# Kernel optimization log

Measured on AMD Instinct MI355X. Metric: run time of the kernel, lower is better.

## Reference

```python
import jax, jax.numpy as jnp
import numpy as np

EPS_RMS = 1e-6  # mmfreelm RMSNorm default eps

def _rmsnorm(x, w):
    var = jnp.mean(x * x, axis=-1, keepdims=True)
    return x * jax.lax.rsqrt(var + EPS_RMS) * w

def _activation_quant(x):
    # per-token absmax int8 quant (BitNet b1.58 activation quant)
    scale = 127.0 / jnp.clip(jnp.max(jnp.abs(x), axis=-1, keepdims=True), 1e-5)
    return jnp.clip(jnp.round(x * scale), -128.0, 127.0) / scale

def _weight_quant(w):
    # ternary quant with global mean-abs scale
    scale = 1.0 / jnp.clip(jnp.mean(jnp.abs(w)), 1e-5)
    return jnp.clip(jnp.round(w * scale), -1.0, 1.0) / scale

def _nm_mask(w, n, m):
    # keep top-n by |w| in every group of m along the input (last) dim
    O, I = w.shape
    g = jnp.abs(w).reshape(-1, m)            # [G, m]
    _, idx = jax.lax.top_k(g, n)             # [G, n]
    rows = jnp.arange(g.shape[0])[:, None]
    mask = jnp.zeros_like(g).at[rows, idx].set(1.0)
    return mask.reshape(O, I)

def setup_inputs() -> dict:
    key = jax.random.key(0)
    k1, k2 = jax.random.split(key)
    B, S, IN, OUT = 4, 2048, 4096, 11008
    x = jax.random.normal(k1, (B, S, IN), dtype=jnp.float32)
    weight = jax.random.normal(k2, (OUT, IN), dtype=jnp.float32) * 0.02
    norm_weight = jnp.ones((IN,), dtype=jnp.float32)
    return {"x": x, "weight": weight, "norm_weight": norm_weight,
            "sparse_n": 2, "sparse_m": 4}

def reference(x, weight, norm_weight, sparse_n, sparse_m):
    x_norm = _rmsnorm(x, norm_weight)
    # STE quantization (forward value == quantized value)
    x_q = x_norm + jax.lax.stop_gradient(_activation_quant(x_norm) - x_norm)
    w_q = weight + jax.lax.stop_gradient(_weight_quant(weight) - weight)
    mask = jax.lax.stop_gradient(_nm_mask(w_q, sparse_n, sparse_m))
    w_sparse = w_q * mask                    # [OUT, IN]
    return jnp.einsum('bsi,oi->bso', x_q, w_sparse)
```

## Files before the change

### kernel.cpp

```cpp
#include <hip/hip_runtime.h>
#include <stdint.h>

#define IN_DIM 4096
#define OUT_DIM 11008
#define TOKENS 8192
#define WN (45088768L)
#define NKT64 64

typedef int int4v __attribute__((ext_vector_type(4)));

__device__ __forceinline__ float bf2f(uint32_t u16) {
  union { uint32_t i; float f; } v; v.i = u16 << 16; return v.f;
}
__device__ __forceinline__ bool probe_bf16(const void* nw) {
  return ((const uint16_t*)nw)[0] == 0x3F80u;
}

__global__ __launch_bounds__(256) void k_wabs(const void* __restrict__ wv,
                                              const void* __restrict__ nwv,
                                              double* __restrict__ partial) {
  const bool b16 = probe_bf16(nwv);
  const long tid = (long)blockIdx.x * 256 + threadIdx.x;
  const long stride = (long)gridDim.x * 256;
  double s = 0.0;
  if (b16) {
    const uint4* w = (const uint4*)wv;
    for (long i = tid; i < WN / 8; i += stride) {
      uint4 v = w[i];
      uint32_t a[4] = {v.x, v.y, v.z, v.w};
      float t = 0.f;
#pragma unroll
      for (int j = 0; j < 4; j++)
        t += fabsf(bf2f(a[j] & 0xffffu)) + fabsf(bf2f(a[j] >> 16));
      s += (double)t;
    }
  } else {
    const float4* w = (const float4*)wv;
    for (long i = tid; i < WN / 4; i += stride) {
      float4 v = w[i];
      s += (double)(fabsf(v.x) + fabsf(v.y) + fabsf(v.z) + fabsf(v.w));
    }
  }
#pragma unroll
  for (int off = 32; off > 0; off >>= 1) s += __shfl_down(s, off);
  __shared__ double sd[4];
  if ((threadIdx.x & 63) == 0) sd[threadIdx.x >> 6] = s;
  __syncthreads();
  if (threadIdx.x == 0) partial[blockIdx.x] = (sd[0] + sd[1]) + (sd[2] + sd[3]);
}

__global__ __launch_bounds__(256) void k_wscale(const double* __restrict__ partial,
                                                float* __restrict__ hdr) {
  double s = 0.0;
  for (int i = threadIdx.x; i < 2048; i += 256) s += partial[i];
#pragma unroll
  for (int off = 32; off > 0; off >>= 1) s += __shfl_down(s, off);
  __shared__ double sd[4];
  if ((threadIdx.x & 63) == 0) sd[threadIdx.x >> 6] = s;
  __syncthreads();
  if (threadIdx.x == 0) {
    double mean = ((sd[0] + sd[1]) + (sd[2] + sd[3])) / (double)WN;
    float meanc = (float)mean;
    if (meanc < 1e-5f) meanc = 1e-5f;
    float wscale = 1.0f / meanc;
    hdr[0] = wscale;
    hdr[1] = 1.0f / wscale;
  }
}

__global__ __launch_bounds__(256) void k_act(const void* __restrict__ xv,
                                             const void* __restrict__ nwv,
                                             int8_t* __restrict__ qxp,
                                             float* __restrict__ invsx) {
  const bool b16 = probe_bf16(nwv);
  const int t = blockIdx.x;
  const int tx = threadIdx.x;
  float xw[16];
  float ss = 0.f, mx = 0.f;
  if (b16) {
    const uint16_t* xr = (const uint16_t*)xv + (long)t * IN_DIM;
    const uint16_t* nw = (const uint16_t*)nwv;
#pragma unroll
    for (int c = 0; c < 2; c++) {
      uint4 vx = ((const uint4*)xr)[tx * 2 + c];
      uint4 vn = ((const uint4*)nw)[tx * 2 + c];
      uint32_t ax[4] = {vx.x, vx.y, vx.z, vx.w};
      uint32_t an[4] = {vn.x, vn.y, vn.z, vn.w};
#pragma unroll
      for (int j = 0; j < 4; j++) {
        float x0 = bf2f(ax[j] & 0xffffu), x1 = bf2f(ax[j] >> 16);
        float n0 = bf2f(an[j] & 0xffffu), n1 = bf2f(an[j] >> 16);
        ss += x0 * x0 + x1 * x1;
        float p0 = x0 * n0, p1 = x1 * n1;
        xw[c * 8 + j * 2]     = p0;
        xw[c * 8 + j * 2 + 1] = p1;
        mx = fmaxf(mx, fmaxf(fabsf(p0), fabsf(p1)));
      }
    }
  } else {
    const float* xr = (const float*)xv + (long)t * IN_DIM;
    const float* nw = (const float*)nwv;
#pragma unroll
    for (int c = 0; c < 4; c++) {
      float4 vx = ((const float4*)xr)[tx * 4 + c];
      float4 vn = ((const float4*)nw)[tx * 4 + c];
      ss += vx.x * vx.x + vx.y * vx.y + vx.z * vx.z + vx.w * vx.w;
      float p0 = vx.x * vn.x, p1 = vx.y * vn.y, p2 = vx.z * vn.z, p3 = vx.w * vn.w;
      xw[c * 4 + 0] = p0; xw[c * 4 + 1] = p1; xw[c * 4 + 2] = p2; xw[c * 4 + 3] = p3;
      mx = fmaxf(mx, fmaxf(fmaxf(fabsf(p0), fabsf(p1)), fmaxf(fabsf(p2), fabsf(p3))));
    }
  }
#pragma unroll
  for (int off = 32; off > 0; off >>= 1) {
    ss += __shfl_down(ss, off);
    mx = fmaxf(mx, __shfl_down(mx, off));
  }
  __shared__ float s_ss[4], s_mx[4];
  __shared__ float bc[1];
  if ((tx & 63) == 0) { s_ss[tx >> 6] = ss; s_mx[tx >> 6] = mx; }
  __syncthreads();
  if (tx == 0) {
    float sst = (s_ss[0] + s_ss[1]) + (s_ss[2] + s_ss[3]);
    float mxt = fmaxf(fmaxf(s_mx[0], s_mx[1]), fmaxf(s_mx[2], s_mx[3]));
    float var = sst / (float)IN_DIM;
    float rms = 1.0f / sqrtf(var + 1e-6f);
    float amax = rms * mxt;
    if (amax < 1e-5f) amax = 1e-5f;
    float scale = 127.0f / amax;
    bc[0] = rms * scale;
    invsx[t] = 1.0f / scale;
  }
  __syncthreads();
  float rsc = bc[0];
  uint32_t pw[4];
#pragma unroll
  for (int d = 0; d < 4; d++) {
    uint32_t v = 0;
#pragma unroll
    for (int j = 0; j < 4; j++) {
      float q = rintf(xw[d * 4 + j] * rsc);
      q = fminf(fmaxf(q, -128.f), 127.f);
      int qi = (int)q;
      v |= ((uint32_t)(qi & 0xff)) << (8 * j);
    }
    pw[d] = v;
  }
  uint4 st; st.x = pw[0]; st.y = pw[1]; st.z = pw[2]; st.w = pw[3];
  const long u4 = (((long)(t >> 7) * 64 + (tx >> 2)) * 8 + ((t >> 4) & 7)) * 64
                + (t & 15) + (tx & 3) * 16;
  ((uint4*)qxp)[u4] = st;
}

__global__ __launch_bounds__(256) void k_wq(const void* __restrict__ wv,
                                            const void* __restrict__ nwv,
                                            const float* __restrict__ hdr,
                                            int8_t* __restrict__ qwp) {
  const bool b16 = probe_bf16(nwv);
  const int o = blockIdx.x;
  const int tx = threadIdx.x;
  const float wscale = hdr[0];
  float f[16];
  if (b16) {
    const uint4* w = (const uint4*)wv;
#pragma unroll
    for (int c = 0; c < 2; ++c) {
      uint4 v = w[(long)o * 512 + tx * 2 + c];
      uint32_t a[4] = {v.x, v.y, v.z, v.w};
#pragma unroll
      for (int j = 0; j < 4; ++j) {
        f[c * 8 + j * 2]     = bf2f(a[j] & 0xffffu);
        f[c * 8 + j * 2 + 1] = bf2f(a[j] >> 16);
      }
    }
  } else {
    const float4* w = (const float4*)wv;
#pragma unroll
    for (int c = 0; c < 4; ++c) {
      float4 v = w[(long)o * 1024 + tx * 4 + c];
      f[c * 4 + 0] = v.x; f[c * 4 + 1] = v.y; f[c * 4 + 2] = v.z; f[c * 4 + 3] = v.w;
    }
  }
  int q[16];
#pragma unroll
  for (int j = 0; j < 16; ++j) {
    float qf = rintf(f[j] * wscale);
    qf = fminf(fmaxf(qf, -1.f), 1.f);
    q[j] = (int)qf;
  }
#pragma unroll
  for (int g = 0; g < 4; ++g) {
    int cnt = 0;
#pragma unroll
    for (int j = 0; j < 4; ++j) {
      int idx = g * 4 + j;
      if (q[idx] != 0) { cnt++; if (cnt > 2) q[idx] = 0; }
    }
  }
  uint32_t pw[4];
#pragma unroll
  for (int d = 0; d < 4; ++d) {
    uint32_t v = 0;
#pragma unroll
    for (int j = 0; j < 4; ++j) v |= ((uint32_t)(q[d * 4 + j] & 0xff)) << (8 * j);
    pw[d] = v;
  }
  uint4 st; st.x = pw[0]; st.y = pw[1]; st.z = pw[2]; st.w = pw[3];
  const long u4 = (((long)(o >> 6) * 64 + (tx >> 2)) * 4 + ((o >> 4) & 3)) * 64
                + (o & 15) + (tx & 3) * 16;
  ((uint4*)qwp)[u4] = st;
}

__global__ __launch_bounds__(512, 2) void k_gemm(const int8_t* __restrict__ qxp,
                                                 const int8_t* __restrict__ qwp,
                                                 const float* __restrict__ invsx,
                                                 const float* __restrict__ hdr,
                                                 float* __restrict__ out) {
  const int tx = threadIdx.x;
  const int wave = tx >> 6, lane = tx & 63;
  const int wr = wave >> 2, wc = wave & 3;
  const int fr = lane & 15;

  const int bid = blockIdx.x;
  const int swz = (bid & 7) * 172 + (bid >> 3);
  const int bm = swz & 31, bn = swz >> 5;
  const int m0 = bm * 256, n0 = bn * 256;

  const int4v* pA = (const int4v*)qxp + (long)(bm * 2 + wr) * (64 * 8 * 64) + lane;
  const int4v* pB = (const int4v*)qwp + (long)(bn * 4 + wc) * (64 * 4 * 64) + lane;

  int4v acc[8][4];
#pragma unroll
  for (int mi = 0; mi < 8; ++mi)
#pragma unroll
    for (int ni = 0; ni < 4; ++ni) {
      acc[mi][ni][0] = 0; acc[mi][ni][1] = 0; acc[mi][ni][2] = 0; acc[mi][ni][3] = 0;
    }

  int4v a[8], b0[4], b1[4];
#pragma unroll
  for (int ni = 0; ni < 4; ++ni) b0[ni] = pB[(long)ni * 64];
#pragma unroll
  for (int mi = 0; mi < 8; ++mi) a[mi] = pA[(long)mi * 64];

#define BODY(T, BCUR, BNXT)                                               \
  {                                                                       \
    const long tn = ((T) + 1 < NKT64) ? (T) + 1 : 0;                      \
    _Pragma("unroll") for (int ni = 0; ni < 4; ++ni)                      \
        BNXT[ni] = pB[(tn * 4 + ni) * 64];                                \
    _Pragma("unroll") for (int mi = 0; mi < 8; ++mi) {                    \
      _Pragma("unroll") for (int ni = 0; ni < 4; ++ni)                    \
          acc[mi][ni] = __builtin_amdgcn_mfma_i32_16x16x64_i8(            \
              a[mi], BCUR[ni], acc[mi][ni], 0, 0, 0);                     \
      a[mi] = pA[(tn * 8 + mi) * 64];                                     \
    }                                                                     \
  }

  for (int t = 0; t < NKT64; t += 2) {
    BODY(t, b0, b1);
    BODY(t + 1, b1, b0);
  }
#undef BODY

  const float winv = hdr[1];
#pragma unroll
  for (int mi = 0; mi < 8; ++mi) {
    const int rbase = m0 + wr * 128 + mi * 16 + (lane >> 4) * 4;
#pragma unroll
    for (int r = 0; r < 4; ++r) {
      const int trow = rbase + r;
      const float fs = invsx[trow] * winv;
      const long ob = (long)trow * OUT_DIM + n0 + wc * 64 + fr;
#pragma unroll
      for (int ni = 0; ni < 4; ++ni) {
        out[ob + ni * 16] = (float)acc[mi][ni][r] * fs;
      }
    }
  }
}

extern "C" void kernel_launch(void* const* d_in, const int* in_sizes, int n_in,
                              void* d_out, int out_size, void* d_ws, size_t ws_size,
                              hipStream_t stream) {
  const void* x  = d_in[0];
  const void* w  = d_in[1];
  const void* nw = d_in[2];
  float* out = (float*)d_out;

  char* ws = (char*)d_ws;
  float*  hdr     = (float*)ws;
  double* partial = (double*)(ws + 1024);
  float*  invsx   = (float*)(ws + 20480);
  int8_t* qxp     = (int8_t*)(ws + (1L << 20));
  int8_t* qwp     = (int8_t*)(ws + 36L * (1L << 20));

  hipLaunchKernelGGL(k_wabs,   dim3(2048),    dim3(256), 0, stream, w, nw, partial);
  hipLaunchKernelGGL(k_wscale, dim3(1),       dim3(256), 0, stream, partial, hdr);
  hipLaunchKernelGGL(k_act,    dim3(TOKENS),  dim3(256), 0, stream, x, nw, qxp, invsx);
  hipLaunchKernelGGL(k_wq,     dim3(OUT_DIM), dim3(256), 0, stream, w, nw, hdr, qwp);
  hipLaunchKernelGGL(k_gemm,   dim3(32 * 43), dim3(512), 0, stream,
                     qxp, qwp, invsx, hdr, out);
}
```

Measured before the change: 737.4 us.

## Stage activation tiles through LDS with direct global-to-LDS loads

Activations are now written row-major, and the GEMM stages each 256x64 A tile into double-buffered shared memory using global_load_lds with an XOR swizzle. All four column waves then share the tile instead of each reloading its own A fragments from global memory. The change cuts redundant global traffic for A and adds s_setprio around the MFMA block. In exchange it adds a __syncthreads per k-step and 32KB of LDS per block, which could limit occupancy at 2 blocks per CU.

```diff
diff --git a/kernel.cpp b/kernel.cpp
--- a/kernel.cpp
+++ b/kernel.cpp
@@ -8,6 +8,8 @@
 #define NKT64 64
 
 typedef int int4v __attribute__((ext_vector_type(4)));
+#define AS1 __attribute__((address_space(1)))
+#define AS3 __attribute__((address_space(3)))
 
 __device__ __forceinline__ float bf2f(uint32_t u16) {
   union { uint32_t i; float f; } v; v.i = u16 << 16; return v.f;
@@ -70,7 +72,7 @@
 
 __global__ __launch_bounds__(256) void k_act(const void* __restrict__ xv,
                                              const void* __restrict__ nwv,
-                                             int8_t* __restrict__ qxp,
+                                             int8_t* __restrict__ qx,
                                              float* __restrict__ invsx) {
   const bool b16 = probe_bf16(nwv);
   const int t = blockIdx.x;
@@ -146,9 +148,7 @@
     pw[d] = v;
   }
   uint4 st; st.x = pw[0]; st.y = pw[1]; st.z = pw[2]; st.w = pw[3];
-  const long u4 = (((long)(t >> 7) * 64 + (tx >> 2)) * 8 + ((t >> 4) & 7)) * 64
-                + (t & 15) + (tx & 3) * 16;
-  ((uint4*)qxp)[u4] = st;
+  ((uint4*)(qx + (long)t * IN_DIM))[tx] = st;
 }
 
 __global__ __launch_bounds__(256) void k_wq(const void* __restrict__ wv,
@@ -210,22 +210,46 @@
   ((uint4*)qwp)[u4] = st;
 }
 
-__global__ __launch_bounds__(512, 2) void k_gemm(const int8_t* __restrict__ qxp,
+__global__ __launch_bounds__(512, 2) void k_gemm(const int8_t* __restrict__ qx,
                                                  const int8_t* __restrict__ qwp,
                                                  const float* __restrict__ invsx,
                                                  const float* __restrict__ hdr,
                                                  float* __restrict__ out) {
+  __shared__ __align__(16) int8_t sA[2][256 * 64];
+
   const int tx = threadIdx.x;
   const int wave = tx >> 6, lane = tx & 63;
   const int wr = wave >> 2, wc = wave & 3;
   const int fr = lane & 15;
+  const int fg = lane >> 4;
 
   const int bid = blockIdx.x;
   const int swz = (bid & 7) * 172 + (bid >> 3);
   const int bm = swz & 31, bn = swz >> 5;
   const int m0 = bm * 256, n0 = bn * 256;
 
-  const int4v* pA = (const int4v*)qxp + (long)(bm * 2 + wr) * (64 * 8 * 64) + lane;
+  const int srow = tx >> 2;
+  const int scol = ((tx & 3) ^ ((srow >> 1) & 3)) * 16;
+  const int8_t* gA = qx + (long)(m0 + srow) * IN_DIM + scol;
+  int8_t* const sA0 = &sA[0][0];
+
+  auto stageA = [&](int t) {
+    if (t >= NKT64) return;
+    int8_t* bA = sA0 + (t & 1) * 16384;
+    const long ko = (long)t * 64;
+    __builtin_amdgcn_global_load_lds(
+        (const AS1 void*)(gA + ko), (AS3 void*)(bA + wave * 1024), 16, 0, 0);
+    __builtin_amdgcn_global_load_lds(
+        (const AS1 void*)(gA + ko + 128L * IN_DIM), (AS3 void*)(bA + 8192 + wave * 1024), 16, 0, 0);
+  };
+
+  int offA[8];
+#pragma unroll
+  for (int mi = 0; mi < 8; ++mi) {
+    const int row = wr * 128 + mi * 16 + fr;
+    offA[mi] = row * 64 + ((fg ^ ((row >> 1) & 3)) * 16);
+  }
+
   const int4v* pB = (const int4v*)qwp + (long)(bn * 4 + wc) * (64 * 4 * 64) + lane;
 
   int4v acc[8][4];
@@ -236,23 +260,29 @@
       acc[mi][ni][0] = 0; acc[mi][ni][1] = 0; acc[mi][ni][2] = 0; acc[mi][ni][3] = 0;
     }
 
-  int4v a[8], b0[4], b1[4];
+  stageA(0);
+  int4v b0[4], b1[4];
 #pragma unroll
   for (int ni = 0; ni < 4; ++ni) b0[ni] = pB[(long)ni * 64];
-#pragma unroll
-  for (int mi = 0; mi < 8; ++mi) a[mi] = pA[(long)mi * 64];
-
-#define BODY(T, BCUR, BNXT)                                               \
+  __syncthreads();
+
+#define BODY(T, BC, BN)                                                   \
   {                                                                       \
+    stageA((T) + 1);                                                      \
     const long tn = ((T) + 1 < NKT64) ? (T) + 1 : 0;                      \
     _Pragma("unroll") for (int ni = 0; ni < 4; ++ni)                      \
-        BNXT[ni] = pB[(tn * 4 + ni) * 64];                                \
-    _Pragma("unroll") for (int mi = 0; mi < 8; ++mi) {                    \
+        BN[ni] = pB[(tn * 4 + ni) * 64];                                  \
+    const int ofs = ((T) & 1) * 16384;                                    \
+    int4v a_[8];                                                          \
+    _Pragma("unroll") for (int mi = 0; mi < 8; ++mi)                      \
+        a_[mi] = *(const int4v*)(sA0 + ofs + offA[mi]);                   \
+    __builtin_amdgcn_s_setprio(1);                                        \
+    _Pragma("unroll") for (int mi = 0; mi < 8; ++mi)                      \
       _Pragma("unroll") for (int ni = 0; ni < 4; ++ni)                    \
           acc[mi][ni] = __builtin_amdgcn_mfma_i32_16x16x64_i8(            \
-              a[mi], BCUR[ni], acc[mi][ni], 0, 0, 0);                     \
-      a[mi] = pA[(tn * 8 + mi) * 64];                                     \
-    }                                                                     \
+              a_[mi], BC[ni], acc[mi][ni], 0, 0, 0);                      \
+    __builtin_amdgcn_s_setprio(0);                                        \
+    __syncthreads();                                                      \
   }
 
   for (int t = 0; t < NKT64; t += 2) {
@@ -290,13 +320,13 @@
   float*  hdr     = (float*)ws;
   double* partial = (double*)(ws + 1024);
   float*  invsx   = (float*)(ws + 20480);
-  int8_t* qxp     = (int8_t*)(ws + (1L << 20));
+  int8_t* qx      = (int8_t*)(ws + (1L << 20));
   int8_t* qwp     = (int8_t*)(ws + 36L * (1L << 20));
 
   hipLaunchKernelGGL(k_wabs,   dim3(2048),    dim3(256), 0, stream, w, nw, partial);
   hipLaunchKernelGGL(k_wscale, dim3(1),       dim3(256), 0, stream, partial, hdr);
-  hipLaunchKernelGGL(k_act,    dim3(TOKENS),  dim3(256), 0, stream, x, nw, qxp, invsx);
+  hipLaunchKernelGGL(k_act,    dim3(TOKENS),  dim3(256), 0, stream, x, nw, qx, invsx);
   hipLaunchKernelGGL(k_wq,     dim3(OUT_DIM), dim3(256), 0, stream, w, nw, hdr, qwp);
   hipLaunchKernelGGL(k_gemm,   dim3(32 * 43), dim3(512), 0, stream,
-                     qxp, qwp, invsx, hdr, out);
-}
+                     qx, qwp, invsx, hdr, out);
+}
```

Measured after the change: 673.2 us. -8.7%, faster.
